# Kernel tuning notes

Hardware: AMD Instinct MI355X
Metric: run time of the kernel (lower is better)

The kernel has to match this reference:

```python
import jax, jax.numpy as jnp
import numpy as np

EPS = 1e-3  # keras LayerNormalization / tfa GroupNormalization default epsilon

def _ln(x, g, b):
    m = jnp.mean(x, axis=-1, keepdims=True)
    v = jnp.var(x, axis=-1, keepdims=True)
    return (x - m) / jnp.sqrt(v + EPS) * g + b

def _gn(x, g, b, groups):
    B, D = x.shape
    xg = x.reshape(B, groups, -1)
    m = jnp.mean(xg, axis=-1, keepdims=True)
    v = jnp.var(xg, axis=-1, keepdims=True)
    xn = ((xg - m) / jnp.sqrt(v + EPS)).reshape(B, D)
    return xn * g + b

def _bd(x, w, b):
    # block-diagonal dense: w [H, in/H, out/H], b [out]
    B = x.shape[0]; H = w.shape[0]
    y = jnp.einsum('bhi,hio->bho', x.reshape(B, H, -1), w)
    return y.reshape(B, -1) + b

def setup_inputs() -> dict:
    B, D, HID, NH = 4096, 2048, 2048, 8
    UP = int(HID * 4 / 3)  # 2730
    key = jax.random.key(0)
    ks = jax.random.split(key, 32)
    s = 0.02
    bd_in = lambda k: jax.random.normal(k, (NH, D // NH, HID // NH), jnp.float32) * s
    bd_h = lambda k: jax.random.normal(k, (NH, HID // NH, HID // NH), jnp.float32) * s
    return {
        'x': jax.random.normal(ks[0], (B, D), jnp.float32),
        'h_prev': jax.random.normal(ks[1], (B, HID), jnp.float32),
        'c_prev': jax.random.normal(ks[2], (B, HID), jnp.float32),
        'n_prev': jnp.ones((B, HID), jnp.float32),
        'm_prev': jnp.zeros((B, HID), jnp.float32),
        'ln_g': jnp.ones((D,), jnp.float32), 'ln_b': jnp.zeros((D,), jnp.float32),
        'conv_k': jax.random.normal(ks[3], (4, D, 1), jnp.float32) * s,
        'conv_b': jnp.zeros((1,), jnp.float32),
        'Wz_w': bd_in(ks[4]), 'Wz_b': jnp.zeros((HID,), jnp.float32),
        'Wi_w': bd_in(ks[5]), 'Wi_b': jnp.zeros((HID,), jnp.float32),
        'Wf_w': bd_in(ks[6]), 'Wf_b': jnp.zeros((HID,), jnp.float32),
        'Wo_w': bd_in(ks[7]), 'Wo_b': jnp.zeros((HID,), jnp.float32),
        'Rz_w': bd_h(ks[8]), 'Rz_b': jnp.zeros((HID,), jnp.float32),
        'Ri_w': bd_h(ks[9]), 'Ri_b': jnp.zeros((HID,), jnp.float32),
        'Rf_w': bd_h(ks[10]), 'Rf_b': jnp.zeros((HID,), jnp.float32),
        'Ro_w': bd_h(ks[11]), 'Ro_b': jnp.zeros((HID,), jnp.float32),
        'gn_g': jnp.ones((HID,), jnp.float32), 'gn_b': jnp.zeros((HID,), jnp.float32),
        'upL_w': jax.random.normal(ks[12], (HID, UP), jnp.float32) * s,
        'upL_b': jnp.zeros((UP,), jnp.float32),
        'upR_w': jax.random.normal(ks[13], (HID, UP), jnp.float32) * s,
        'upR_b': jnp.zeros((UP,), jnp.float32),
        'down_w': jax.random.normal(ks[14], (UP, D), jnp.float32) * s,
        'down_b': jnp.zeros((D,), jnp.float32),
    }

def reference(x, h_prev, c_prev, n_prev, m_prev, ln_g, ln_b, conv_k, conv_b,
              Wz_w, Wz_b, Wi_w, Wi_b, Wf_w, Wf_b, Wo_w, Wo_b,
              Rz_w, Rz_b, Ri_w, Ri_b, Rf_w, Rf_b, Ro_w, Ro_b,
              gn_g, gn_b, upL_w, upL_b, upR_w, upR_b, down_w, down_b):
    NH = Wz_w.shape[0]
    x_norm = _ln(x, ln_g, ln_b)
    # CausalConv1D on a length-1 time axis: left zero-pad (k-1) means only the
    # last kernel tap sees x_norm -> scalar per sample; broadcast across channels
    conv_scalar = x_norm @ conv_k[-1, :, 0] + conv_b[0]          # [B]
    x_conv = jnp.broadcast_to(jax.nn.silu(conv_scalar)[:, None], x_norm.shape)
    z = jnp.tanh(_bd(x, Wz_w, Wz_b) + _bd(h_prev, Rz_w, Rz_b))
    o = jax.nn.sigmoid(_bd(x, Wo_w, Wo_b) + _bd(h_prev, Ro_w, Ro_b))
    i_tilde = _bd(x_conv, Wi_w, Wi_b) + _bd(h_prev, Ri_w, Ri_b)
    f_tilde = _bd(x_conv, Wf_w, Wf_b) + _bd(h_prev, Rf_w, Rf_b)
    m_t = jnp.maximum(f_tilde + m_prev, i_tilde)                 # stabilizer
    i = jnp.exp(i_tilde - m_t)
    f = jnp.exp(f_tilde + m_prev - m_t)
    c_t = f * c_prev + i * z
    n_t = f * n_prev + i
    h_t = o * c_t / n_t
    out_norm = _gn(h_t, gn_g, gn_b, NH)
    out_left = out_norm @ upL_w + upL_b
    out_right = out_norm @ upR_w + upR_b
    out = (out_left * jax.nn.gelu(out_right, approximate=False)) @ down_w + down_b
    final_output = out + x
    return (final_output, h_t, c_t, n_t, m_t)
```

## Files before the change

kernel.cpp:

```cpp
#include <hip/hip_runtime.h>
#include <hip/hip_bf16.h>

typedef unsigned short u16;
typedef unsigned int u32x4 __attribute__((ext_vector_type(4)));
typedef unsigned short us4 __attribute__((ext_vector_type(4)));
typedef __bf16 bf16x8 __attribute__((ext_vector_type(8)));
typedef float f32x4 __attribute__((ext_vector_type(4)));

__device__ __forceinline__ float b2f(u16 u) {
  union { unsigned int i; float f; } v; v.i = ((unsigned int)u) << 16; return v.f;
}
__device__ __forceinline__ u16 f2b(float f) {
  unsigned int x = __builtin_bit_cast(unsigned int, f);
  unsigned int r = (x + 0x7fffu + ((x >> 16) & 1u)) >> 16;
  return (u16)r;
}

__device__ __forceinline__ void stage16(const u16* g, u16* l) {
  __builtin_amdgcn_global_load_lds((const __attribute__((address_space(1))) void*)g,
                                   (__attribute__((address_space(3))) void*)l,
                                   16, 0, 0);
}

__global__ void cvt_k(const float* __restrict__ in, u16* __restrict__ out, long n) {
  long i = ((long)blockIdx.x * 256 + threadIdx.x) * 4;
  if (i + 3 < n) {
    float4 v = *(const float4*)(in + i);
    out[i] = f2b(v.x); out[i+1] = f2b(v.y); out[i+2] = f2b(v.z); out[i+3] = f2b(v.w);
  } else {
    for (long k = i; k < n; ++k) out[k] = f2b(in[k]);
  }
}

__global__ void transpose_k(const float* __restrict__ in, u16* __restrict__ out,
                            int R, int C, int ldo) {
  __shared__ float t[32][33];
  int c0 = blockIdx.x * 32, r0 = blockIdx.y * 32;
  for (int i = threadIdx.y; i < 32; i += 8) {
    int r = r0 + i, c = c0 + threadIdx.x;
    t[i][threadIdx.x] = (r < R && c < C) ? in[(long)r * C + c] : 0.f;
  }
  __syncthreads();
  for (int i = threadIdx.y; i < 32; i += 8) {
    int c = c0 + i, r = r0 + threadIdx.x;
    if (c < C && r < ldo) out[(long)c * ldo + r] = f2b(t[threadIdx.x][i]);
  }
}

__global__ void transpose6_k(const float* __restrict__ Wz, const float* __restrict__ Wo,
                             const float* __restrict__ Rz, const float* __restrict__ Ro,
                             const float* __restrict__ Ri, const float* __restrict__ Rf,
                             u16* __restrict__ zoW, u16* __restrict__ zoR,
                             u16* __restrict__ irfW) {
  __shared__ float t[32][33];
  int zz = blockIdx.z; int wsel = zz >> 3, h = zz & 7;
  const float* in; u16* outp;
  switch (wsel) {
    case 0: in = Wz; outp = zoW;          break;
    case 1: in = Wo; outp = zoW + 65536;  break;
    case 2: in = Rz; outp = zoR;          break;
    case 3: in = Ro; outp = zoR + 65536;  break;
    case 4: in = Ri; outp = irfW;         break;
    default: in = Rf; outp = irfW + 65536; break;
  }
  in += (long)h * 65536; outp += (long)h * 131072;
  int c0 = blockIdx.x * 32, r0 = blockIdx.y * 32;
  for (int i = threadIdx.y; i < 32; i += 8)
    t[i][threadIdx.x] = in[(long)(r0 + i) * 256 + c0 + threadIdx.x];
  __syncthreads();
  for (int i = threadIdx.y; i < 32; i += 8)
    outp[(long)(c0 + i) * 256 + r0 + threadIdx.x] = f2b(t[threadIdx.x][i]);
}

__global__ void transpose_up_k(const float* __restrict__ L, const float* __restrict__ R,
                               u16* __restrict__ out) {
  __shared__ float t[32][33];
  const float* in = blockIdx.z ? R : L;
  u16* o = out + (long)blockIdx.z * 2730 * 2048;
  int c0 = blockIdx.x * 32, r0 = blockIdx.y * 32;
  for (int i = threadIdx.y; i < 32; i += 8) {
    int r = r0 + i, c = c0 + threadIdx.x;
    t[i][threadIdx.x] = (c < 2730) ? in[(long)r * 2730 + c] : 0.f;
  }
  __syncthreads();
  for (int i = threadIdx.y; i < 32; i += 8) {
    int c = c0 + i, r = r0 + threadIdx.x;
    if (c < 2730) o[(long)c * 2048 + r] = f2b(t[threadIdx.x][i]);
  }
}

__global__ void colsum2_k(const float* __restrict__ Wi, const float* __restrict__ Wf,
                          float* __restrict__ csi, float* __restrict__ csf) {
  const float* W = blockIdx.y ? Wf : Wi;
  float* outp = blockIdx.y ? csf : csi;
  int bb = blockIdx.x; int h = bb >> 2, cq = bb & 3;
  int t = threadIdx.x;
  int col = cq * 64 + (t & 63);
  int rg = t >> 6;
  const float* p = W + (long)h * 65536 + col;
  float s = 0.f;
  for (int r = rg * 64; r < rg * 64 + 64; ++r) s += p[(long)r * 256];
  __shared__ float red[4][64];
  red[rg][t & 63] = s;
  __syncthreads();
  if (t < 64) outp[h * 256 + cq * 64 + t] = red[0][t] + red[1][t] + red[2][t] + red[3][t];
}

__global__ void ln_conv_k(const float* __restrict__ x, const float* __restrict__ g,
                          const float* __restrict__ bb, const float* __restrict__ ck,
                          const float* __restrict__ cb, float* __restrict__ xc,
                          u16* __restrict__ xb) {
  __shared__ float s1[4], s2[4];
  int b = blockIdx.x, tid = threadIdx.x;
  const float* xr = x + (long)b * 2048;
  u16* xbr = xb + (long)b * 2048;
  float v[8], sum = 0.f, sq = 0.f;
  #pragma unroll
  for (int i = 0; i < 8; ++i) {
    float f = xr[tid + i * 256];
    v[i] = f; sum += f; sq += f * f;
    xbr[tid + i * 256] = f2b(f);
  }
  #pragma unroll
  for (int off = 32; off; off >>= 1) {
    sum += __shfl_down(sum, off, 64);
    sq  += __shfl_down(sq,  off, 64);
  }
  int lane = tid & 63, wv = tid >> 6;
  if (!lane) { s1[wv] = sum; s2[wv] = sq; }
  __syncthreads();
  float tsum = s1[0] + s1[1] + s1[2] + s1[3];
  float tsq  = s2[0] + s2[1] + s2[2] + s2[3];
  float m = tsum * (1.f / 2048.f);
  float var = tsq * (1.f / 2048.f) - m * m;
  float rstd = rsqrtf(var + 1e-3f);
  float dot = 0.f;
  #pragma unroll
  for (int i = 0; i < 8; ++i) {
    int d = tid + i * 256;
    float xn = (v[i] - m) * rstd * g[d] + bb[d];
    dot += xn * ck[3 * 2048 + d];
  }
  #pragma unroll
  for (int off = 32; off; off >>= 1) dot += __shfl_down(dot, off, 64);
  __syncthreads();
  if (!lane) s1[wv] = dot;
  __syncthreads();
  if (tid == 0) {
    float s = s1[0] + s1[1] + s1[2] + s1[3] + cb[0];
    xc[b] = s / (1.f + expf(-s));
  }
}

template<bool F32OUT>
__global__ __launch_bounds__(256) void gemm_bt(
    const u16* __restrict__ A1, long lda1, long sA1,
    const u16* __restrict__ Bt1, long ldb1, long sB1,
    const u16* __restrict__ A2, long lda2, long sA2,
    const u16* __restrict__ Bt2, long ldb2, long sB2,
    int K1, int K2,
    const float* __restrict__ bias,
    const float* __restrict__ res, long ldres,
    void* __restrict__ Cv, long ldc, long sC,
    int M, int N, int nsplit, long off2)
{
  __shared__ u16 As[128][32];
  __shared__ u16 Bs[128][32];
  const int bz = blockIdx.z;
  A1 += (long)bz * sA1; Bt1 += (long)bz * sB1;
  if (A2) { A2 += (long)bz * sA2; Bt2 += (long)bz * sB2; }
  int gx = gridDim.x;
  int lin = blockIdx.y * gx + blockIdx.x;
  int nwg = gx * gridDim.y;
  if ((nwg & 7) == 0) {
    int cpx = nwg >> 3;
    lin = (lin & 7) * cpx + (lin >> 3);
  }
  const int m0 = (lin / gx) * 128, n0 = (lin % gx) * 128;
  const int tid = threadIdx.x;
  const int w = tid >> 6, lane = tid & 63;
  const int lr = lane & 15, quad = lane >> 4;
  const int wrow = (w & 1) * 64, wcol = (w >> 1) * 64;
  const int srow = lane >> 2;
  const int scol = (lane & 3) * 8;
  f32x4 acc[4][4] = {};
  const int KT = K1 + K2;
  for (int kk = 0; kk < KT; kk += 32) {
    const u16 *PA, *PB; long lA, lB; int ko;
    if (kk < K1) { PA = A1; lA = lda1; PB = Bt1; lB = ldb1; ko = kk; }
    else         { PA = A2; lA = lda2; PB = Bt2; lB = ldb2; ko = kk - K1; }
    #pragma unroll
    for (int c = 0; c < 2; ++c) {
      const int r0 = (w * 2 + c) * 16;
      long ar = m0 + r0 + srow; if (ar > (long)M - 1) ar = M - 1;
      long br = n0 + r0 + srow; if (br > (long)N - 1) br = N - 1;
      stage16(PA + ar * lA + ko + scol, &As[r0][0]);
      stage16(PB + br * lB + ko + scol, &Bs[r0][0]);
    }
    asm volatile("s_waitcnt vmcnt(0)" ::: "memory");
    __syncthreads();
    bf16x8 af[4], bfr[4];
    #pragma unroll
    for (int i = 0; i < 4; ++i)
      af[i] = __builtin_bit_cast(bf16x8, *(const u32x4*)&As[wrow + i * 16 + lr][quad * 8]);
    #pragma unroll
    for (int j = 0; j < 4; ++j)
      bfr[j] = __builtin_bit_cast(bf16x8, *(const u32x4*)&Bs[wcol + j * 16 + lr][quad * 8]);
    #pragma unroll
    for (int i = 0; i < 4; ++i)
      #pragma unroll
      for (int j = 0; j < 4; ++j)
        acc[i][j] = __builtin_amdgcn_mfma_f32_16x16x32_bf16(af[i], bfr[j], acc[i][j], 0, 0, 0);
    __syncthreads();
  }
  #pragma unroll
  for (int i = 0; i < 4; ++i) {
    #pragma unroll
    for (int r = 0; r < 4; ++r) {
      int row = m0 + wrow + i * 16 + quad * 4 + r;
      if (row >= M) continue;
      #pragma unroll
      for (int j = 0; j < 4; ++j) {
        int col = n0 + wcol + j * 16 + lr;
        if (col >= N) continue;
        float v = acc[i][j][r];
        if (bias) v += bias[col];
        if (res)  v += res[(long)row * ldres + col];
        long e = (long)bz * sC + (long)row * ldc + col;
        if (col >= nsplit) e += off2;
        if (F32OUT) ((float*)Cv)[e] = v;
        else        ((u16*)Cv)[e] = f2b(v);
      }
    }
  }
}

__global__ void gates_gn_k(
    const u16* __restrict__ zpre, const u16* __restrict__ opre,
    const u16* __restrict__ ri,   const u16* __restrict__ rf,
    const float* __restrict__ xc, const float* __restrict__ csi, const float* __restrict__ csf,
    const float* __restrict__ Wz_b, const float* __restrict__ Rz_b,
    const float* __restrict__ Wi_b, const float* __restrict__ Ri_b,
    const float* __restrict__ Wf_b, const float* __restrict__ Rf_b,
    const float* __restrict__ Wo_b, const float* __restrict__ Ro_b,
    const float* __restrict__ c_prev, const float* __restrict__ n_prev,
    const float* __restrict__ m_prev,
    const float* __restrict__ gn_g, const float* __restrict__ gn_b,
    float* __restrict__ h_out, float* __restrict__ c_out,
    float* __restrict__ n_out, float* __restrict__ m_out,
    u16* __restrict__ onorm)
{
  int t = threadIdx.x;
  long base = (long)blockIdx.x * 256 + t * 4;
  int j = (int)(base & 2047);
  long b = base >> 11;
  us4 z4 = *(const us4*)(zpre + base);
  us4 o4 = *(const us4*)(opre + base);
  us4 i4 = *(const us4*)(ri + base);
  us4 f4 = *(const us4*)(rf + base);
  f32x4 cp = *(const f32x4*)(c_prev + base);
  f32x4 np = *(const f32x4*)(n_prev + base);
  f32x4 mp = *(const f32x4*)(m_prev + base);
  float xcb = xc[b];
  float ht[4]; f32x4 ho, co, no, mo;
  float sum = 0.f, sq = 0.f;
  #pragma unroll
  for (int e = 0; e < 4; ++e) {
    int jj = j + e;
    float zp = b2f(z4[e]) + Wz_b[jj] + Rz_b[jj];
    float op = b2f(o4[e]) + Wo_b[jj] + Ro_b[jj];
    float it = xcb * csi[jj] + Wi_b[jj] + b2f(i4[e]) + Ri_b[jj];
    float ft = xcb * csf[jj] + Wf_b[jj] + b2f(f4[e]) + Rf_b[jj];
    float z = tanhf(zp);
    float o = 1.f / (1.f + expf(-op));
    float mt = fmaxf(ft + mp[e], it);
    float ii = expf(it - mt), ff = expf(ft + mp[e] - mt);
    float ct = ff * cp[e] + ii * z;
    float nt = ff * np[e] + ii;
    float h = o * ct / nt;
    ht[e] = h; ho[e] = h; co[e] = ct; no[e] = nt; mo[e] = mt;
    sum += h; sq += h * h;
  }
  *(f32x4*)(h_out + base) = ho;
  *(f32x4*)(c_out + base) = co;
  *(f32x4*)(n_out + base) = no;
  *(f32x4*)(m_out + base) = mo;
  #pragma unroll
  for (int off = 32; off; off >>= 1) {
    sum += __shfl_down(sum, off, 64);
    sq  += __shfl_down(sq,  off, 64);
  }
  sum = __shfl(sum, 0, 64); sq = __shfl(sq, 0, 64);
  float m = sum * (1.f / 256.f);
  float var = sq * (1.f / 256.f) - m * m;
  float rstd = rsqrtf(var + 1e-3f);
  us4 og;
  #pragma unroll
  for (int e = 0; e < 4; ++e)
    og[e] = f2b((ht[e] - m) * rstd * gn_g[j + e] + gn_b[j + e]);
  *(us4*)(onorm + base) = og;
}

__global__ void combine_k(u16* __restrict__ buf,
                          const float* __restrict__ lb, const float* __restrict__ rb) {
  int i4 = blockIdx.x * 256 + threadIdx.x;
  if (i4 >= 688) return;
  int col = i4 * 4;
  long base = (long)blockIdx.y * 5504 + col;
  us4 l4 = *(const us4*)(buf + base);
  us4 r4 = *(const us4*)(buf + base + 2752);
  us4 a;
  #pragma unroll
  for (int e = 0; e < 4; ++e) {
    int c = col + e;
    if (c >= 2730) { a[e] = 0; continue; }
    float l = b2f(l4[e]) + lb[c];
    float r = b2f(r4[e]) + rb[c];
    float gel = 0.5f * r * (1.f + erff(r * 0.70710678118654752f));
    a[e] = f2b(l * gel);
  }
  *(us4*)(buf + base) = a;
}

extern "C" void kernel_launch(void* const* d_in, const int* in_sizes, int n_in,
                              void* d_out, int out_size, void* d_ws, size_t ws_size,
                              hipStream_t stream)
{
  const float* x      = (const float*)d_in[0];
  const float* h_prev = (const float*)d_in[1];
  const float* c_prev = (const float*)d_in[2];
  const float* n_prev = (const float*)d_in[3];
  const float* m_prev = (const float*)d_in[4];
  const float* ln_g   = (const float*)d_in[5];
  const float* ln_b   = (const float*)d_in[6];
  const float* conv_k = (const float*)d_in[7];
  const float* conv_b = (const float*)d_in[8];
  const float* Wz_w = (const float*)d_in[9];  const float* Wz_b = (const float*)d_in[10];
  const float* Wi_w = (const float*)d_in[11]; const float* Wi_b = (const float*)d_in[12];
  const float* Wf_w = (const float*)d_in[13]; const float* Wf_b = (const float*)d_in[14];
  const float* Wo_w = (const float*)d_in[15]; const float* Wo_b = (const float*)d_in[16];
  const float* Rz_w = (const float*)d_in[17]; const float* Rz_b = (const float*)d_in[18];
  const float* Ri_w = (const float*)d_in[19]; const float* Ri_b = (const float*)d_in[20];
  const float* Rf_w = (const float*)d_in[21]; const float* Rf_b = (const float*)d_in[22];
  const float* Ro_w = (const float*)d_in[23]; const float* Ro_b = (const float*)d_in[24];
  const float* gn_g = (const float*)d_in[25]; const float* gn_b = (const float*)d_in[26];
  const float* upL_w = (const float*)d_in[27]; const float* upL_b = (const float*)d_in[28];
  const float* upR_w = (const float*)d_in[29]; const float* upR_b = (const float*)d_in[30];
  const float* down_w = (const float*)d_in[31]; const float* down_b = (const float*)d_in[32];

  char* ws = (char*)d_ws;
  u16* zoW   = (u16*)(ws + 0);
  u16* zoR   = (u16*)(ws + 2097152);
  u16* irfW  = (u16*)(ws + 4194304);
  u16* upLT  = (u16*)(ws + 6291456);
  u16* downT = (u16*)(ws + 28655616);
  float* csi = (float*)(ws + 39945216);
  float* csf = (float*)(ws + 39953408);
  float* xc  = (float*)(ws + 39961600);
  u16* zpre  = (u16*)(ws + 39980032);
  u16* opre  = (u16*)(ws + 56757248);
  u16* ri    = (u16*)(ws + 73534464);
  u16* rf    = (u16*)(ws + 90311680);
  u16* xb    = (u16*)(ws + 107088896);
  u16* hb    = (u16*)(ws + 123866112);
  u16* onorm = xb;
  u16* updub = zpre;

  float* out   = (float*)d_out;
  float* final_o = out;
  float* hout  = out + 8388608;
  float* cout  = out + 16777216;
  float* nout  = out + 25165824;
  float* mout  = out + 33554432;

  const long GATE_OFF2 = 8388608 - 256;
  const int  NOSPLIT = 1 << 30;

  dim3 tb(32, 8);
  cvt_k<<<8192, 256, 0, stream>>>(h_prev, hb, 8388608);
  ln_conv_k<<<4096, 256, 0, stream>>>(x, ln_g, ln_b, conv_k, conv_b, xc, xb);
  transpose6_k<<<dim3(8, 8, 48), tb, 0, stream>>>(Wz_w, Wo_w, Rz_w, Ro_w, Ri_w, Rf_w,
                                                  zoW, zoR, irfW);
  transpose_up_k<<<dim3(86, 64, 2), tb, 0, stream>>>(upL_w, upR_w, upLT);
  transpose_k<<<dim3(64, 86, 1), tb, 0, stream>>>(down_w, downT, 2730, 2048, 2752);
  colsum2_k<<<dim3(32, 2), 256, 0, stream>>>(Wi_w, Wf_w, csi, csf);
  gemm_bt<false><<<dim3(4, 32, 8), 256, 0, stream>>>(
      xb, 2048, 256, zoW, 256, 131072, hb, 2048, 256, zoR, 256, 131072,
      256, 256, nullptr, nullptr, 0, zpre, 2048, 256, 4096, 512, 256, GATE_OFF2);
  gemm_bt<false><<<dim3(4, 32, 8), 256, 0, stream>>>(
      hb, 2048, 256, irfW, 256, 131072, nullptr, 0, 0, nullptr, 0, 0,
      256, 0, nullptr, nullptr, 0, ri, 2048, 256, 4096, 512, 256, GATE_OFF2);
  gates_gn_k<<<32768, 64, 0, stream>>>(zpre, opre, ri, rf, xc, csi, csf,
      Wz_b, Rz_b, Wi_b, Ri_b, Wf_b, Rf_b, Wo_b, Ro_b,
      c_prev, n_prev, m_prev, gn_g, gn_b, hout, cout, nout, mout, onorm);
  gemm_bt<false><<<dim3(43, 32, 1), 256, 0, stream>>>(
      onorm, 2048, 0, upLT, 2048, 0, nullptr, 0, 0, nullptr, 0, 0,
      2048, 0, nullptr, nullptr, 0, updub, 5504, 0, 4096, 5460, 2730, 22);
  combine_k<<<dim3(3, 4096), 256, 0, stream>>>(updub, upL_b, upR_b);
  gemm_bt<true><<<dim3(16, 32, 1), 256, 0, stream>>>(
      updub, 5504, 0, downT, 2752, 0, nullptr, 0, 0, nullptr, 0, 0,
      2752, 0, down_b, x, 2048, final_o, 2048, 0, 4096, 2048, NOSPLIT, 0);
}
```

Measured before the change: 869.8 us.

## Add 256x256-tile triple-buffered GEMM kernel for up and down projections

Adds a new GEMM kernel with 256x256 output tiles, 512 threads (8 waves, each computing a 128x64 sub-tile), a three-stage LDS ring buffer filled by direct global-to-LDS loads, XCD-aware block remapping, and s_setprio around the MFMA bursts. The up-projection and down-projection GEMMs now use it instead of the 128-tile kernel. The aim is more operand reuse per LDS load and better overlap of loads with MFMA work. The trade-off is higher register and LDS pressure (96 KB of LDS), fewer workgroups (352 and 128), and more tile-quantization waste on N=5460.

New measurement: 920.9 us. +5.9%, slower.

```diff
diff --git a/kernel.cpp b/kernel.cpp
--- a/kernel.cpp
+++ b/kernel.cpp
@@ -227,6 +227,107 @@
         if (bias) v += bias[col];
         if (res)  v += res[(long)row * ldres + col];
         long e = (long)bz * sC + (long)row * ldc + col;
+        if (col >= nsplit) e += off2;
+        if (F32OUT) ((float*)Cv)[e] = v;
+        else        ((u16*)Cv)[e] = f2b(v);
+      }
+    }
+  }
+}
+
+template<bool F32OUT>
+__global__ __launch_bounds__(512) void gemm256(
+    const u16* __restrict__ A, long lda,
+    const u16* __restrict__ Bt, long ldb,
+    int K,
+    const float* __restrict__ bias,
+    const float* __restrict__ res, long ldres,
+    void* __restrict__ Cv, long ldc,
+    int M, int N, int nsplit, long off2)
+{
+  __shared__ __align__(16) u16 lds[3][2][8192];
+  int gx = gridDim.x;
+  int lin = blockIdx.y * gx + blockIdx.x;
+  int nwg = gx * gridDim.y;
+  int cpx = nwg >> 3;
+  lin = (lin & 7) * cpx + (lin >> 3);
+  const int m0 = (lin / gx) * 256, n0 = (lin % gx) * 256;
+  const int tid = threadIdx.x;
+  const int wv = tid >> 6, lane = tid & 63;
+  const int wr = wv >> 2, wc = wv & 3;
+  const int lr = lane & 15, quad = lane >> 4;
+  const int srow = lane >> 2;
+  const int scg  = (lane & 3) ^ ((lane >> 2) & 3);
+  const int cphys = (quad ^ (lr & 3)) * 8;
+  const int NT = K >> 5;
+  f32x4 acc[8][4] = {};
+
+  auto stage = [&](int t, int b) {
+    int k0 = t << 5;
+    #pragma unroll
+    for (int q = 0; q < 2; ++q) {
+      long ar = m0 + q * 128 + wv * 16 + srow;
+      stage16(A + ar * lda + k0 + scg * 8, &lds[b][0][q * 4096 + wv * 512]);
+    }
+    #pragma unroll
+    for (int q = 0; q < 2; ++q) {
+      long br = n0 + q * 128 + wv * 16 + srow;
+      if (br > (long)N - 1) br = N - 1;
+      stage16(Bt + br * ldb + k0 + scg * 8, &lds[b][1][q * 4096 + wv * 512]);
+    }
+  };
+
+  stage(0, 0);
+  if (NT > 1) stage(1, 1);
+  for (int t = 0; t < NT; ++t) {
+    if (t + 1 < NT) asm volatile("s_waitcnt vmcnt(4)" ::: "memory");
+    else            asm volatile("s_waitcnt vmcnt(0)" ::: "memory");
+    __builtin_amdgcn_s_barrier();
+    __builtin_amdgcn_sched_barrier(0);
+    if (t + 2 < NT) stage(t + 2, (t + 2) % 3);
+    const u16* Ab = &lds[t % 3][0][0];
+    const u16* Bb = &lds[t % 3][1][0];
+    bf16x8 bf[4], af[4];
+    #pragma unroll
+    for (int j = 0; j < 4; ++j)
+      bf[j] = __builtin_bit_cast(bf16x8,
+          *(const u32x4*)&Bb[(wc * 64 + j * 16 + lr) * 32 + cphys]);
+    #pragma unroll
+    for (int i = 0; i < 4; ++i)
+      af[i] = __builtin_bit_cast(bf16x8,
+          *(const u32x4*)&Ab[(wr * 128 + i * 16 + lr) * 32 + cphys]);
+    __builtin_amdgcn_s_setprio(1);
+    #pragma unroll
+    for (int i = 0; i < 4; ++i)
+      #pragma unroll
+      for (int j = 0; j < 4; ++j)
+        acc[i][j] = __builtin_amdgcn_mfma_f32_16x16x32_bf16(af[i], bf[j], acc[i][j], 0, 0, 0);
+    __builtin_amdgcn_s_setprio(0);
+    #pragma unroll
+    for (int i = 0; i < 4; ++i)
+      af[i] = __builtin_bit_cast(bf16x8,
+          *(const u32x4*)&Ab[(wr * 128 + (i + 4) * 16 + lr) * 32 + cphys]);
+    __builtin_amdgcn_s_setprio(1);
+    #pragma unroll
+    for (int i = 0; i < 4; ++i)
+      #pragma unroll
+      for (int j = 0; j < 4; ++j)
+        acc[i + 4][j] = __builtin_amdgcn_mfma_f32_16x16x32_bf16(af[i], bf[j], acc[i + 4][j], 0, 0, 0);
+    __builtin_amdgcn_s_setprio(0);
+  }
+  #pragma unroll
+  for (int i = 0; i < 8; ++i) {
+    #pragma unroll
+    for (int r = 0; r < 4; ++r) {
+      int row = m0 + wr * 128 + i * 16 + quad * 4 + r;
+      #pragma unroll
+      for (int j = 0; j < 4; ++j) {
+        int col = n0 + wc * 64 + j * 16 + lr;
+        if (col >= N) continue;
+        float v = acc[i][j][r];
+        if (bias) v += bias[col];
+        if (res)  v += res[(long)row * ldres + col];
+        long e = (long)row * ldc + col;
         if (col >= nsplit) e += off2;
         if (F32OUT) ((float*)Cv)[e] = v;
         else        ((u16*)Cv)[e] = f2b(v);
@@ -393,11 +494,11 @@
   gates_gn_k<<<32768, 64, 0, stream>>>(zpre, opre, ri, rf, xc, csi, csf,
       Wz_b, Rz_b, Wi_b, Ri_b, Wf_b, Rf_b, Wo_b, Ro_b,
       c_prev, n_prev, m_prev, gn_g, gn_b, hout, cout, nout, mout, onorm);
-  gemm_bt<false><<<dim3(43, 32, 1), 256, 0, stream>>>(
-      onorm, 2048, 0, upLT, 2048, 0, nullptr, 0, 0, nullptr, 0, 0,
-      2048, 0, nullptr, nullptr, 0, updub, 5504, 0, 4096, 5460, 2730, 22);
+  gemm256<false><<<dim3(22, 16), 512, 0, stream>>>(
+      onorm, 2048, upLT, 2048, 2048,
+      nullptr, nullptr, 0, updub, 5504, 4096, 5460, 2730, 22);
   combine_k<<<dim3(3, 4096), 256, 0, stream>>>(updub, upL_b, upR_b);
-  gemm_bt<true><<<dim3(16, 32, 1), 256, 0, stream>>>(
-      updub, 5504, 0, downT, 2752, 0, nullptr, 0, 0, nullptr, 0, 0,
-      2752, 0, down_b, x, 2048, final_o, 2048, 0, 4096, 2048, NOSPLIT, 0);
-}
+  gemm256<true><<<dim3(8, 16), 512, 0, stream>>>(
+      updub, 5504, downT, 2752, 2752,
+      down_b, x, 2048, final_o, 2048, 4096, 2048, NOSPLIT, 0);
+}
```
